# Performance work log

Measured on AMD Instinct MI355X. Metric: run time of the kernel, lower is better.

Reference implementation:

```python
import jax, jax.numpy as jnp
import numpy as np

M, K, N = 64, 4096, 14336


def setup_inputs() -> dict:
    key = jax.random.key(0)
    k1, k2, k3, k4, k5 = jax.random.split(key, 5)
    x = jax.random.normal(k1, (M, K), dtype=jnp.float32)
    # int8-valued weights stored as int32 (values in [-128, 128))
    weight = jax.random.randint(k2, (K, N), -128, 128, dtype=jnp.int32)
    # per-channel dequant params (one per output channel N)
    antiquant_scale = jax.random.uniform(k3, (N,), dtype=jnp.float32, minval=0.001, maxval=0.02)
    antiquant_offset = jax.random.normal(k4, (N,), dtype=jnp.float32)
    bias = jax.random.normal(k5, (N,), dtype=jnp.float32)
    return {"x": x, "weight": weight, "antiquant_scale": antiquant_scale,
            "antiquant_offset": antiquant_offset, "bias": bias}


def reference(x, weight, antiquant_scale, antiquant_offset, bias):
    # npu_weight_quant_batchmatmul, per-channel antiquant, no output quant:
    # out = x @ ((weight + antiquant_offset) * antiquant_scale) + bias
    w_deq = (weight.astype(x.dtype) + antiquant_offset[None, :]) * antiquant_scale[None, :]  # [K, N]
    out = jnp.einsum('mk,kn->mn', x, w_deq) + bias[None, :]  # [M, N]
    return out
```

## Files before the change

kernel.cpp:

```cpp
#include <hip/hip_runtime.h>
#include <hip/hip_bf16.h>

#define M_DIM 64
#define K_DIM 4096
#define N_DIM 14336
#define TN 32
#define TK 64
#define KITERS (K_DIM / TK)

typedef __attribute__((ext_vector_type(8))) short bf16x8;
typedef __attribute__((ext_vector_type(4))) float f32x4;

__global__ void prep_split(const float* __restrict__ x,
                           __hip_bfloat16* __restrict__ xh,
                           __hip_bfloat16* __restrict__ xl) {
  int tg = blockIdx.x * blockDim.x + threadIdx.x;
  int m = tg & 63;
  int kb = tg >> 6;
  const float* xp = x + m * K_DIM + kb * 8;
  int o = kb * (M_DIM * 8) + m * 8;
#pragma unroll
  for (int j = 0; j < 8; ++j) {
    float v = xp[j];
    __hip_bfloat16 h = __float2bfloat16(v);
    float r = v - __bfloat162float(h);
    xh[o + j] = h;
    xl[o + j] = __float2bfloat16(r);
  }
}

__global__ void rowsum_k(const float* __restrict__ x, float* __restrict__ rs) {
  int m = blockIdx.x;
  int t = threadIdx.x;
  float s = 0.f;
  for (int k = t; k < K_DIM; k += 256) s += x[m * K_DIM + k];
#pragma unroll
  for (int off = 32; off > 0; off >>= 1) s += __shfl_down(s, off, 64);
  __shared__ float red[4];
  if ((t & 63) == 0) red[t >> 6] = s;
  __syncthreads();
  if (t == 0) rs[m] = red[0] + red[1] + red[2] + red[3];
}

__global__ __launch_bounds__(256) void wqmm(
    const int* __restrict__ W, const __hip_bfloat16* __restrict__ xh,
    const __hip_bfloat16* __restrict__ xl, const float* __restrict__ rowsum,
    const float* __restrict__ scale, const float* __restrict__ offset,
    const float* __restrict__ bias, float* __restrict__ out) {
  __shared__ __align__(16) unsigned short bsh[2][TN][72];

  const int t = threadIdx.x;
  const int lane = t & 63;
  const int wv = t >> 6;
  const int quad = lane >> 4;
  const int lnk = lane & 15;
  const int nblk = blockIdx.x * TN;

  f32x4 acc0 = {0.f, 0.f, 0.f, 0.f};
  f32x4 acc1 = {0.f, 0.f, 0.f, 0.f};

  const int kl0 = t >> 3;
  const int kl1 = kl0 + 32;
  const int nl = (t & 7) * 4;

  int4 wreg[2];

  const int mrow = wv * 16 + lnk;
  const __hip_bfloat16* xh_m = xh + mrow * 8;
  const __hip_bfloat16* xl_m = xl + mrow * 8;

#define STAGE_LOAD(k0)                                                      \
  do {                                                                      \
    wreg[0] = *(const int4*)(W + (size_t)((k0) + kl0) * N_DIM + nblk + nl); \
    wreg[1] = *(const int4*)(W + (size_t)((k0) + kl1) * N_DIM + nblk + nl); \
  } while (0)

#define STAGE_WRITE(p)                                              \
  do {                                                              \
    _Pragma("unroll") for (int c = 0; c < 2; ++c) {                 \
      int kl = c ? kl1 : kl0;                                       \
      int vals[4] = {wreg[c].x, wreg[c].y, wreg[c].z, wreg[c].w};   \
      _Pragma("unroll") for (int i = 0; i < 4; ++i) {               \
        float f = (float)vals[i];              \
        bsh[p][nl + i][kl] =                                        \
            (unsigned short)(__float_as_uint(f) >> 16);  \
      }                                                             \
    }                                                               \
  } while (0)

  STAGE_LOAD(0);
  STAGE_WRITE(0);
  int p = 0;

  for (int it = 0; it < KITERS; ++it) {
    __syncthreads();
    if (it + 1 < KITERS) STAGE_LOAD((it + 1) * TK);

    const int kb0 = it * (TK / 8);
#pragma unroll
    for (int ks = 0; ks < 2; ++ks) {
      const int kb = kb0 + ks * 4 + quad;
      bf16x8 ah = *(const bf16x8*)(xh_m + kb * (M_DIM * 8));
      bf16x8 al = *(const bf16x8*)(xl_m + kb * (M_DIM * 8));
      bf16x8 b0 = *(const bf16x8*)&bsh[p][lnk][ks * 32 + quad * 8];
      bf16x8 b1 = *(const bf16x8*)&bsh[p][16 + lnk][ks * 32 + quad * 8];
      acc0 = __builtin_amdgcn_mfma_f32_16x16x32_bf16(ah, b0, acc0, 0, 0, 0);
      acc0 = __builtin_amdgcn_mfma_f32_16x16x32_bf16(al, b0, acc0, 0, 0, 0);
      acc1 = __builtin_amdgcn_mfma_f32_16x16x32_bf16(ah, b1, acc1, 0, 0, 0);
      acc1 = __builtin_amdgcn_mfma_f32_16x16x32_bf16(al, b1, acc1, 0, 0, 0);
    }

    if (it + 1 < KITERS) STAGE_WRITE(p ^ 1);
    p ^= 1;
  }

#pragma unroll
  for (int nbi = 0; nbi < 2; ++nbi) {
    int n = nblk + nbi * 16 + lnk;
    float s = scale[n];
    float so = s * offset[n];
    float bi = bias[n];
    f32x4 a = nbi ? acc1 : acc0;
#pragma unroll
    for (int r = 0; r < 4; ++r) {
      int m = wv * 16 + quad * 4 + r;
      out[(size_t)m * N_DIM + n] = a[r] * s + so * rowsum[m] + bi;
    }
  }
}

extern "C" void kernel_launch(void* const* d_in, const int* in_sizes, int n_in,
                              void* d_out, int out_size, void* d_ws,
                              size_t ws_size, hipStream_t stream) {
  const float* x = (const float*)d_in[0];
  const int* W = (const int*)d_in[1];
  const float* scale = (const float*)d_in[2];
  const float* offset = (const float*)d_in[3];
  const float* bias = (const float*)d_in[4];
  float* out = (float*)d_out;

  __hip_bfloat16* xh = (__hip_bfloat16*)d_ws;
  __hip_bfloat16* xl = xh + (size_t)M_DIM * K_DIM;
  float* rowsum = (float*)(xl + (size_t)M_DIM * K_DIM);

  prep_split<<<128, 256, 0, stream>>>(x, xh, xl);
  rowsum_k<<<64, 256, 0, stream>>>(x, rowsum);
  wqmm<<<N_DIM / TN, 256, 0, stream>>>(W, xh, xl, rowsum, scale, offset, bias,
                                       out);
}
```

Baseline: 349.0 us.

## Split K across blocks with atomic reduction and direct-register weight dequant

Restructures the GEMM into a split-K scheme: each block owns 256 output columns and a 256-wide K slice, keeps the whole activation slice in shared memory, and loads int32 weights straight into registers, converting them to bf16 fragments without an LDS round trip. Partial sums are combined with float atomics into an output zeroed by a new kernel, and bias and offset are added only by the first slice. The prep kernel now truncates instead of rounding to bf16 for the high part and writes vectorized. The aim is more parallelism and better use of weight bandwidth, paid for with atomic traffic, an extra zeroing pass, non-deterministic summation order, and heavy register pressure from 64 accumulators.

```diff
diff --git a/kernel.cpp b/kernel.cpp
--- a/kernel.cpp
+++ b/kernel.cpp
@@ -4,9 +4,11 @@
 #define M_DIM 64
 #define K_DIM 4096
 #define N_DIM 14336
-#define TN 32
-#define TK 64
-#define KITERS (K_DIM / TK)
+#define KSPLIT 16
+#define KSLICE (K_DIM / KSPLIT)
+#define NB_BLK 256
+#define NBLKS (N_DIM / NB_BLK)
+#define CHUNKS (KSLICE / 32)
 
 typedef __attribute__((ext_vector_type(8))) short bf16x8;
 typedef __attribute__((ext_vector_type(4))) float f32x4;
@@ -15,18 +17,21 @@
                            __hip_bfloat16* __restrict__ xh,
                            __hip_bfloat16* __restrict__ xl) {
   int tg = blockIdx.x * blockDim.x + threadIdx.x;
-  int m = tg & 63;
-  int kb = tg >> 6;
+  int kb = tg & 511;
+  int m = tg >> 9;
   const float* xp = x + m * K_DIM + kb * 8;
-  int o = kb * (M_DIM * 8) + m * 8;
+  unsigned short hs[8], ls[8];
 #pragma unroll
   for (int j = 0; j < 8; ++j) {
     float v = xp[j];
-    __hip_bfloat16 h = __float2bfloat16(v);
-    float r = v - __bfloat162float(h);
-    xh[o + j] = h;
-    xl[o + j] = __float2bfloat16(r);
+    unsigned hv = __float_as_uint(v) & 0xFFFF0000u;
+    float r = v - __uint_as_float(hv);
+    hs[j] = (unsigned short)(hv >> 16);
+    ls[j] = (unsigned short)(__float_as_uint(r) >> 16);
   }
+  int o = kb * (M_DIM * 8) + m * 8;
+  *(uint4*)((unsigned short*)xh + o) = *(uint4*)hs;
+  *(uint4*)((unsigned short*)xl + o) = *(uint4*)ls;
 }
 
 __global__ void rowsum_k(const float* __restrict__ x, float* __restrict__ rs) {
@@ -42,89 +47,96 @@
   if (t == 0) rs[m] = red[0] + red[1] + red[2] + red[3];
 }
 
+__global__ void zero_out(float* __restrict__ out) {
+  int i = blockIdx.x * blockDim.x + threadIdx.x;
+  ((float4*)out)[i] = make_float4(0.f, 0.f, 0.f, 0.f);
+}
+
 __global__ __launch_bounds__(256) void wqmm(
     const int* __restrict__ W, const __hip_bfloat16* __restrict__ xh,
     const __hip_bfloat16* __restrict__ xl, const float* __restrict__ rowsum,
     const float* __restrict__ scale, const float* __restrict__ offset,
     const float* __restrict__ bias, float* __restrict__ out) {
-  __shared__ __align__(16) unsigned short bsh[2][TN][72];
+  __shared__ __align__(16) unsigned short ash[2][KSLICE / 8][M_DIM * 8];
 
   const int t = threadIdx.x;
   const int lane = t & 63;
   const int wv = t >> 6;
   const int quad = lane >> 4;
   const int lnk = lane & 15;
-  const int nblk = blockIdx.x * TN;
+  const int nb = blockIdx.x % NBLKS;
+  const int ks = blockIdx.x / NBLKS;
+  const int k0 = ks * KSLICE;
+  const int nbase = nb * NB_BLK + wv * 64;
 
-  f32x4 acc0 = {0.f, 0.f, 0.f, 0.f};
-  f32x4 acc1 = {0.f, 0.f, 0.f, 0.f};
+  {
+    const uint4* srch = (const uint4*)((const unsigned short*)xh + k0 * 64);
+    const uint4* srcl = (const uint4*)((const unsigned short*)xl + k0 * 64);
+    uint4* dsth = (uint4*)&ash[0][0][0];
+    uint4* dstl = (uint4*)&ash[1][0][0];
+#pragma unroll
+    for (int i = 0; i < 8; ++i) {
+      dsth[t + i * 256] = srch[t + i * 256];
+      dstl[t + i * 256] = srcl[t + i * 256];
+    }
+  }
+  __syncthreads();
 
-  const int kl0 = t >> 3;
-  const int kl1 = kl0 + 32;
-  const int nl = (t & 7) * 4;
+  f32x4 acc[4][4] = {};
 
-  int4 wreg[2];
+  const int* wp = W + (size_t)(k0 + quad * 8) * N_DIM + nbase + lnk;
 
-  const int mrow = wv * 16 + lnk;
-  const __hip_bfloat16* xh_m = xh + mrow * 8;
-  const __hip_bfloat16* xl_m = xl + mrow * 8;
-
-#define STAGE_LOAD(k0)                                                      \
-  do {                                                                      \
-    wreg[0] = *(const int4*)(W + (size_t)((k0) + kl0) * N_DIM + nblk + nl); \
-    wreg[1] = *(const int4*)(W + (size_t)((k0) + kl1) * N_DIM + nblk + nl); \
-  } while (0)
-
-#define STAGE_WRITE(p)                                              \
-  do {                                                              \
-    _Pragma("unroll") for (int c = 0; c < 2; ++c) {                 \
-      int kl = c ? kl1 : kl0;                                       \
-      int vals[4] = {wreg[c].x, wreg[c].y, wreg[c].z, wreg[c].w};   \
-      _Pragma("unroll") for (int i = 0; i < 4; ++i) {               \
-        float f = (float)vals[i];              \
-        bsh[p][nl + i][kl] =                                        \
-            (unsigned short)(__float_as_uint(f) >> 16);  \
-      }                                                             \
-    }                                                               \
-  } while (0)
-
-  STAGE_LOAD(0);
-  STAGE_WRITE(0);
-  int p = 0;
-
-  for (int it = 0; it < KITERS; ++it) {
-    __syncthreads();
-    if (it + 1 < KITERS) STAGE_LOAD((it + 1) * TK);
-
-    const int kb0 = it * (TK / 8);
+#pragma unroll 2
+  for (int c = 0; c < CHUNKS; ++c) {
+    int raw[4][8];
 #pragma unroll
-    for (int ks = 0; ks < 2; ++ks) {
-      const int kb = kb0 + ks * 4 + quad;
-      bf16x8 ah = *(const bf16x8*)(xh_m + kb * (M_DIM * 8));
-      bf16x8 al = *(const bf16x8*)(xl_m + kb * (M_DIM * 8));
-      bf16x8 b0 = *(const bf16x8*)&bsh[p][lnk][ks * 32 + quad * 8];
-      bf16x8 b1 = *(const bf16x8*)&bsh[p][16 + lnk][ks * 32 + quad * 8];
-      acc0 = __builtin_amdgcn_mfma_f32_16x16x32_bf16(ah, b0, acc0, 0, 0, 0);
-      acc0 = __builtin_amdgcn_mfma_f32_16x16x32_bf16(al, b0, acc0, 0, 0, 0);
-      acc1 = __builtin_amdgcn_mfma_f32_16x16x32_bf16(ah, b1, acc1, 0, 0, 0);
-      acc1 = __builtin_amdgcn_mfma_f32_16x16x32_bf16(al, b1, acc1, 0, 0, 0);
+    for (int j = 0; j < 8; ++j) {
+      const int* pj = wp + (size_t)(c * 32 + j) * N_DIM;
+#pragma unroll
+      for (int f = 0; f < 4; ++f) raw[f][j] = pj[f * 16];
     }
-
-    if (it + 1 < KITERS) STAGE_WRITE(p ^ 1);
-    p ^= 1;
+    bf16x8 bfr[4];
+#pragma unroll
+    for (int f = 0; f < 4; ++f) {
+      union { int i4[4]; bf16x8 v; } u;
+#pragma unroll
+      for (int wd = 0; wd < 4; ++wd) {
+        unsigned lo = __float_as_uint((float)raw[f][2 * wd]);
+        unsigned hi = __float_as_uint((float)raw[f][2 * wd + 1]);
+        u.i4[wd] = (int)((lo >> 16) | (hi & 0xFFFF0000u));
+      }
+      bfr[f] = u.v;
+    }
+#pragma unroll
+    for (int mt = 0; mt < 4; ++mt) {
+      bf16x8 ah = *(const bf16x8*)&ash[0][c * 4 + quad][(mt * 16 + lnk) * 8];
+      bf16x8 al = *(const bf16x8*)&ash[1][c * 4 + quad][(mt * 16 + lnk) * 8];
+#pragma unroll
+      for (int f = 0; f < 4; ++f) {
+        acc[mt][f] =
+            __builtin_amdgcn_mfma_f32_16x16x32_bf16(ah, bfr[f], acc[mt][f], 0, 0, 0);
+        acc[mt][f] =
+            __builtin_amdgcn_mfma_f32_16x16x32_bf16(al, bfr[f], acc[mt][f], 0, 0, 0);
+      }
+    }
   }
 
+  const int mb = quad * 4;
 #pragma unroll
-  for (int nbi = 0; nbi < 2; ++nbi) {
-    int n = nblk + nbi * 16 + lnk;
+  for (int f = 0; f < 4; ++f) {
+    int n = nbase + f * 16 + lnk;
     float s = scale[n];
     float so = s * offset[n];
     float bi = bias[n];
-    f32x4 a = nbi ? acc1 : acc0;
 #pragma unroll
-    for (int r = 0; r < 4; ++r) {
-      int m = wv * 16 + quad * 4 + r;
-      out[(size_t)m * N_DIM + n] = a[r] * s + so * rowsum[m] + bi;
+    for (int mt = 0; mt < 4; ++mt) {
+#pragma unroll
+      for (int r = 0; r < 4; ++r) {
+        int m = mt * 16 + mb + r;
+        float v = acc[mt][f][r] * s;
+        if (ks == 0) v += so * rowsum[m] + bi;
+        unsafeAtomicAdd(out + (size_t)m * N_DIM + n, v);
+      }
     }
   }
 }
@@ -143,8 +155,9 @@
   __hip_bfloat16* xl = xh + (size_t)M_DIM * K_DIM;
   float* rowsum = (float*)(xl + (size_t)M_DIM * K_DIM);
 
+  zero_out<<<M_DIM * N_DIM / 4 / 256, 256, 0, stream>>>(out);
   prep_split<<<128, 256, 0, stream>>>(x, xh, xl);
   rowsum_k<<<64, 256, 0, stream>>>(x, rowsum);
-  wqmm<<<N_DIM / TN, 256, 0, stream>>>(W, xh, xl, rowsum, scale, offset, bias,
-                                       out);
+  wqmm<<<NBLKS * KSPLIT, 256, 0, stream>>>(W, xh, xl, rowsum, scale, offset,
+                                           bias, out);
 }
```

Result: slower. 363.2 us (+4.0%).
